# Optimization experiments

Measured on AMD Instinct MI355X. Metric: run time of the kernel, lower is better.

The kernel has to match this reference:

```python
import jax, jax.numpy as jnp
import numpy as np
import math

D_MODEL = 1024
N_HEADS = 16
D_HEAD = 64
D_MLP = 4096
N_LAYERS = 12
INIT_STD = 0.02
EPS = 1e-5
BATCH = 2
SEQ = 2048


def setup_inputs() -> dict:
    key = jax.random.key(0)
    ks = jax.random.split(key, 8)
    attn_std = INIT_STD
    proj_std = INIT_STD / math.sqrt(2 * N_LAYERS)
    return {
        "resid_pre": jax.random.normal(ks[0], (BATCH, SEQ, D_MODEL), jnp.float32),
        "ln1_w": jnp.ones((D_MODEL,), jnp.float32),
        "ln1_b": jnp.zeros((D_MODEL,), jnp.float32),
        "W_Q": attn_std * jax.random.normal(ks[1], (N_HEADS, D_MODEL, D_HEAD), jnp.float32),
        "b_Q": jnp.zeros((N_HEADS, D_HEAD), jnp.float32),
        "W_K": attn_std * jax.random.normal(ks[2], (N_HEADS, D_MODEL, D_HEAD), jnp.float32),
        "b_K": jnp.zeros((N_HEADS, D_HEAD), jnp.float32),
        "W_V": attn_std * jax.random.normal(ks[3], (N_HEADS, D_MODEL, D_HEAD), jnp.float32),
        "b_V": jnp.zeros((N_HEADS, D_HEAD), jnp.float32),
        "W_O": proj_std * jax.random.normal(ks[4], (N_HEADS, D_HEAD, D_MODEL), jnp.float32),
        "b_O": jnp.zeros((D_MODEL,), jnp.float32),
        "ln2_w": jnp.ones((D_MODEL,), jnp.float32),
        "ln2_b": jnp.zeros((D_MODEL,), jnp.float32),
        "W_in": INIT_STD * jax.random.normal(ks[5], (D_MODEL, D_MLP), jnp.float32),
        "b_in": jnp.zeros((D_MLP,), jnp.float32),
        "W_out": proj_std * jax.random.normal(ks[6], (D_MLP, D_MODEL), jnp.float32),
        "b_out": jnp.zeros((D_MODEL,), jnp.float32),
    }


def _layernorm(x, w, b):
    mean = x.mean(-1, keepdims=True)
    var = x.var(-1, keepdims=True)  # unbiased=False
    return (x - mean) / jnp.sqrt(var + EPS) * w + b


def _attention(x, W_Q, b_Q, W_K, b_K, W_V, b_V, W_O, b_O):
    # x: [b, s, d]; W_*: [h, d, k]
    q = jnp.einsum('bsd,hdk->bshk', x, W_Q) + b_Q
    k = jnp.einsum('bsd,hdk->bshk', x, W_K) + b_K
    v = jnp.einsum('bsd,hdk->bshk', x, W_V) + b_V
    scores = jnp.einsum('bqhk,bshk->bhqs', q, k) / math.sqrt(D_HEAD)
    seq = x.shape[1]
    causal = jnp.tril(jnp.ones((seq, seq), bool))
    scores = jnp.where(causal, scores, -jnp.inf)
    pattern = jax.nn.softmax(scores, axis=-1)
    z = jnp.einsum('bhqs,bshk->bqhk', pattern, v)
    return jnp.einsum('bqhk,hkd->bqd', z, W_O) + b_O


def reference(resid_pre, ln1_w, ln1_b, W_Q, b_Q, W_K, b_K, W_V, b_V, W_O, b_O,
              ln2_w, ln2_b, W_in, b_in, W_out, b_out):
    attn_out = _attention(_layernorm(resid_pre, ln1_w, ln1_b),
                          W_Q, b_Q, W_K, b_K, W_V, b_V, W_O, b_O)
    resid_mid = resid_pre + attn_out
    h = _layernorm(resid_mid, ln2_w, ln2_b)
    mlp_out = jnp.matmul(jax.nn.relu(jnp.matmul(h, W_in) + b_in), W_out) + b_out
    return resid_mid + mlp_out
```

## Files before the change

### kernel.cpp

```cpp
#include <hip/hip_runtime.h>
#include <stdint.h>


typedef unsigned short u16;
typedef __bf16 bf16x8 __attribute__((ext_vector_type(8)));
typedef __bf16 bf16x4 __attribute__((ext_vector_type(4)));
typedef __bf16 bf16x2 __attribute__((ext_vector_type(2)));
typedef short  s16x4  __attribute__((ext_vector_type(4)));
typedef float  f32x4  __attribute__((ext_vector_type(4)));

#define QSCALE 0.18033688011112042f

__device__ __forceinline__ float bf2f(unsigned int u) {
  union { unsigned int u; float f; } v; v.u = u << 16; return v.f;
}
__device__ __forceinline__ u16 f2bf(float f) {
  union { float f; unsigned int u; } v; v.f = f;
  unsigned int r = v.u + 0x7FFFu + ((v.u >> 16) & 1u);
  return (u16)(r >> 16);
}
__device__ __forceinline__ unsigned pkbf(float lo, float hi) {
#if __has_builtin(__builtin_amdgcn_cvt_pk_bf16_f32)
  bf16x2 t = __builtin_amdgcn_cvt_pk_bf16_f32(lo, hi);
  return __builtin_bit_cast(unsigned, t);
#else
  return (unsigned)f2bf(lo) | ((unsigned)f2bf(hi) << 16);
#endif
}
__device__ __forceinline__ float loadf(const void* p, size_t i, int isf) {
  return isf ? ((const float*)p)[i] : bf2f(((const u16*)p)[i]);
}

__device__ __forceinline__ f32x4 mfma16(s16x4 a, s16x4 b, f32x4 c) {
#if __has_builtin(__builtin_amdgcn_mfma_f32_16x16x16_bf16)
  return __builtin_amdgcn_mfma_f32_16x16x16_bf16(
      __builtin_bit_cast(bf16x4, a), __builtin_bit_cast(bf16x4, b), c, 0, 0, 0);
#else
  return __builtin_amdgcn_mfma_f32_16x16x16bf16_1k(a, b, c, 0, 0, 0);
#endif
}

__global__ __launch_bounds__(256) void detect_dtype(
    const unsigned int* __restrict__ x, int* __restrict__ flag) {
  __shared__ int cnt;
  if (threadIdx.x == 0) cnt = 0;
  __syncthreads();
  int c = 0;
  for (int i = threadIdx.x; i < 512; i += 256) {
    unsigned int e = (x[i] >> 23) & 0xFFu;
    if (e >= 97u && e <= 157u) c++;
  }
  atomicAdd(&cnt, c);
  __syncthreads();
  if (threadIdx.x == 0) *flag = (cnt > 384) ? 1 : 0;
}

__global__ __launch_bounds__(256) void pack_qkv_tiled(
    const int* __restrict__ flagp,
    const void* __restrict__ Wq, const void* __restrict__ Wk, const void* __restrict__ Wv,
    u16* __restrict__ WT) {
  __shared__ float t[64][65];
  const int isf = *flagp;
  const int tid = threadIdx.x;
  const int mh = blockIdx.y;
  const int mat = mh >> 4, h = mh & 15;
  const int d0 = blockIdx.x << 6;
  const void* src = (mat == 0) ? Wq : (mat == 1) ? Wk : Wv;
  const float scale = (mat == 0) ? QSCALE : 1.f;
  const int lane = tid & 63, rr = tid >> 6;
  const size_t sbase = ((size_t)h << 16) + lane;
#pragma unroll
  for (int i = 0; i < 16; i++) {
    int d = i * 4 + rr;
    t[d][lane] = loadf(src, sbase + (size_t)(d0 + d) * 64, isf) * scale;
  }
  __syncthreads();
#pragma unroll
  for (int i = 0; i < 16; i++) {
    int k = i * 4 + rr;
    WT[((size_t)((mat << 10) + (h << 6) + k) << 10) + d0 + lane] = f2bf(t[lane][k]);
  }
}

__global__ __launch_bounds__(256) void transpose_tiled(
    const int* __restrict__ flagp, const void* __restrict__ src,
    u16* __restrict__ dst, int R, int C) {
  __shared__ float t[64][65];
  const int isf = *flagp;
  const int tid = threadIdx.x;
  const int c0 = blockIdx.x << 6, r0 = blockIdx.y << 6;
  const int lane = tid & 63, rr = tid >> 6;
#pragma unroll
  for (int i = 0; i < 16; i++) {
    int r = i * 4 + rr;
    t[r][lane] = loadf(src, (size_t)(r0 + r) * C + c0 + lane, isf);
  }
  __syncthreads();
#pragma unroll
  for (int i = 0; i < 16; i++) {
    int c = i * 4 + rr;
    dst[(size_t)(c0 + c) * R + r0 + lane] = f2bf(t[lane][c]);
  }
}

__global__ __launch_bounds__(256) void pack_biases(
    const int* __restrict__ flagp,
    const void* bq, const void* bk, const void* bv,
    const void* bO, const void* bin, const void* bout,
    float* __restrict__ out) {
  const int isf = *flagp;
  int i = blockIdx.x * 256 + threadIdx.x;
  float v;
  if (i < 1024)      v = loadf(bq,   i,        isf) * QSCALE;
  else if (i < 2048) v = loadf(bk,   i - 1024, isf);
  else if (i < 3072) v = loadf(bv,   i - 2048, isf);
  else if (i < 4096) v = loadf(bO,   i - 3072, isf);
  else if (i < 8192) v = loadf(bin,  i - 4096, isf);
  else               v = loadf(bout, i - 8192, isf);
  out[i] = v;
}

template<int SRC>
__global__ __launch_bounds__(256) void ln_fwd(
    const int* __restrict__ flagp, const void* __restrict__ xin,
    const void* __restrict__ w, const void* __restrict__ b,
    u16* __restrict__ out) {
  const int isf = *flagp;
  const int row = blockIdx.x, tid = threadIdx.x;
  const int col = tid << 2;
  const size_t base = ((size_t)row << 10) + col;
  float v[4];
#pragma unroll
  for (int i = 0; i < 4; i++)
    v[i] = (SRC == 1) ? ((const float*)xin)[base + i] : loadf(xin, base + i, isf);
  float s  = v[0] + v[1] + v[2] + v[3];
  float ss = v[0]*v[0] + v[1]*v[1] + v[2]*v[2] + v[3]*v[3];
#pragma unroll
  for (int mk = 32; mk >= 1; mk >>= 1) {
    s  += __shfl_xor(s,  mk, 64);
    ss += __shfl_xor(ss, mk, 64);
  }
  __shared__ float red[8];
  if ((tid & 63) == 0) { red[tid >> 6] = s; red[4 + (tid >> 6)] = ss; }
  __syncthreads();
  float S  = red[0] + red[1] + red[2] + red[3];
  float SS = red[4] + red[5] + red[6] + red[7];
  float mean = S * (1.f / 1024.f);
  float var  = SS * (1.f / 1024.f) - mean * mean;
  float rstd = rsqrtf(var + 1e-5f);
  u16 e[4];
#pragma unroll
  for (int i = 0; i < 4; i++) {
    float wv = loadf(w, col + i, isf);
    float bv = loadf(b, col + i, isf);
    e[i] = f2bf((v[i] - mean) * rstd * wv + bv);
  }
  uint2 o;
  o.x = (unsigned)e[0] | ((unsigned)e[1] << 16);
  o.y = (unsigned)e[2] | ((unsigned)e[3] << 16);
  *(uint2*)(out + base) = o;
}

template<int MODE, int TM>
__global__ __launch_bounds__(256) void gemm_bt(
    const int* __restrict__ flagp,
    const u16* __restrict__ A, const u16* __restrict__ BT,
    const float* __restrict__ bias, const void* __restrict__ resid,
    void* __restrict__ out, void* __restrict__ out2, void* __restrict__ out3,
    int M, int N, int K, int SHL) {
  constexpr int WR = TM / 32;
  __shared__ u16 as[TM * 32];
  __shared__ u16 bs[128 * 32];
  int isf = 0;
  if (MODE == 2 || MODE == 3) isf = *flagp;
  const int Lb = blockIdx.x;
  const int xcd = Lb & 7, sidx = Lb >> 3;
  const int SH = 1 << SHL;
  const int by = xcd * SH + (sidx & (SH - 1));
  const int bx = sidx >> SHL;
  const int tid = threadIdx.x;
  const int L = tid & 63, w = tid >> 6;
  const int wm = (w >> 1) * (TM >> 1), wn = (w & 1) << 6;
  const int row0 = by * TM, col0 = bx << 7;
  const int m = L & 15, quad = L >> 4;

  f32x4 zero4 = {0.f, 0.f, 0.f, 0.f};
  f32x4 acc[WR][4];
#pragma unroll
  for (int i = 0; i < WR; i++)
#pragma unroll
    for (int j = 0; j < 4; j++) acc[i][j] = zero4;

  const int tm = tid >> 2;
  const int tk = (tid & 3) << 3;
  const u16* Ag  = A  + (size_t)(row0 + tm) * K + tk;
  const u16* Ag2 = Ag + (size_t)64 * K;
  const u16* Bg  = BT + (size_t)(col0 + tm) * K + tk;
  const u16* Bg2 = Bg + (size_t)64 * K;
  u16* asl  = &as[tid * 8];
  u16* asl2 = &as[2048 + tid * 8];
  u16* bsl  = &bs[tid * 8];
  u16* bsl2 = &bs[2048 + tid * 8];

  const int aoff = (wm + m) * 32 + quad * 8;
  const int boff = (wn + m) * 32 + quad * 8;

  int4 ar0, ar1, br0, br1;
  ar0 = *(const int4*)Ag;
  if (TM == 128) ar1 = *(const int4*)Ag2;
  br0 = *(const int4*)Bg;
  br1 = *(const int4*)Bg2;

  for (int kk = 0; kk < K; kk += 32) {
    __syncthreads();
    *(int4*)asl = ar0;
    if (TM == 128) *(int4*)asl2 = ar1;
    *(int4*)bsl = br0;
    *(int4*)bsl2 = br1;
    __syncthreads();
    if (kk + 32 < K) {
      ar0 = *(const int4*)(Ag + kk + 32);
      if (TM == 128) ar1 = *(const int4*)(Ag2 + kk + 32);
      br0 = *(const int4*)(Bg + kk + 32);
      br1 = *(const int4*)(Bg2 + kk + 32);
    }
    bf16x8 af[WR], bfr[4];
#pragma unroll
    for (int i = 0; i < WR; i++) af[i]  = *(const bf16x8*)&as[aoff + i * 512];
#pragma unroll
    for (int j = 0; j < 4; j++) bfr[j] = *(const bf16x8*)&bs[boff + j * 512];
#pragma unroll
    for (int i = 0; i < WR; i++)
#pragma unroll
      for (int j = 0; j < 4; j++)
        acc[i][j] = __builtin_amdgcn_mfma_f32_16x16x32_bf16(af[i], bfr[j], acc[i][j], 0, 0, 0);
  }

#pragma unroll
  for (int j = 0; j < 4; j++) {
    const int col = col0 + wn + j * 16 + m;
    const float bval = bias[col];
    if (MODE == 4) {
      const int sel = col >> 10;
      const int hh  = (col >> 6) & 15;
      const int f   = col & 63;
#pragma unroll
      for (int i = 0; i < WR; i++) {
        const int rowb = row0 + wm + i * 16 + quad * 4;
        if (sel < 2) {
          u16* dst = (u16*)(sel ? out2 : out);
#pragma unroll
          for (int r = 0; r < 4; r++)
            dst[((((size_t)hh << 12) + rowb + r) << 6) + f] = f2bf(acc[i][j][r] + bval);
        } else {
          uint2 o;
          o.x = pkbf(acc[i][j][0] + bval, acc[i][j][1] + bval);
          o.y = pkbf(acc[i][j][2] + bval, acc[i][j][3] + bval);
          *(uint2*)&((u16*)out3)[(((size_t)hh * 64 + f) << 12) + rowb] = o;
        }
      }
    } else {
#pragma unroll
      for (int i = 0; i < WR; i++) {
        const int rowb = row0 + wm + i * 16 + quad * 4;
#pragma unroll
        for (int r = 0; r < 4; r++) {
          float vv = acc[i][j][r] + bval;
          size_t idx = (size_t)(rowb + r) * N + col;
          if (MODE == 1) {
            ((u16*)out)[idx] = f2bf(fmaxf(vv, 0.f));
          } else if (MODE == 2) {
            ((float*)out)[idx] = vv + loadf(resid, idx, isf);
          } else if (MODE == 3) {
            float o = vv + ((const float*)resid)[idx];
            if (isf) ((float*)out)[idx] = o;
            else     ((u16*)out)[idx]   = f2bf(o);
          }
        }
      }
    }
  }
}

__global__ __launch_bounds__(256, 3) void attn_part(
    const u16* __restrict__ qh, const u16* __restrict__ kh,
    const u16* __restrict__ vT, u16* __restrict__ Opart,
    float* __restrict__ stats) {
  const int combo = blockIdx.x;
  const int qt = blockIdx.y;
  const int ci = blockIdx.z;
  const int q0 = qt << 6;
  const int nc = (q0 + 64 + 511) >> 9;
  if (ci >= nc) return;
  const int k_lo = ci << 9;
  const int k_hi = min(k_lo + 512, q0 + 64);
  const int nsteps = (k_hi - k_lo + 127) >> 7;

  __shared__ u16 kS[128 * 72];
  __shared__ u16 vS[64 * 136];
  const int tid = threadIdx.x, L = tid & 63, w = tid >> 6;
  const int m = L & 15, quad = L >> 4;
  const int h = combo >> 1, b = combo & 1;
  const size_t tb = (size_t)b * 2048;
  const size_t hbase = (size_t)h * 4096;
  const int qg = q0 + w * 16 + m;

  bf16x8 qb0, qb1;
  {
    const u16* qp = qh + ((hbase + tb + (size_t)qg) << 6) + quad * 8;
    qb0 = *(const bf16x8*)qp;
    qb1 = *(const bf16x8*)(qp + 32);
  }

  f32x4 zero4 = {0.f, 0.f, 0.f, 0.f};
  f32x4 O[4];
#pragma unroll
  for (int ft = 0; ft < 4; ft++) O[ft] = zero4;
  float mrow = -30000.f, lrow = 0.f;

  const int krow[4] = { (0*256+tid) >> 3, (1*256+tid) >> 3, (2*256+tid) >> 3, (3*256+tid) >> 3 };
  const int kc = tid & 7;
  const int vf[4] = { (0*256+tid) >> 4, (1*256+tid) >> 4, (2*256+tid) >> 4, (3*256+tid) >> 4 };
  const int vc = tid & 15;
  const int vq = (vc & 1) << 1;
  const int vk4 = (vc >> 1) << 2;
  const int vc0 = (vq << 5) + vk4;
  const int vc1 = ((vq + 1) << 5) + vk4;

  int4 kr[4], vr[4];
#pragma unroll
  for (int i = 0; i < 4; i++) {
    kr[i] = *(const int4*)(kh + ((hbase + tb + k_lo + krow[i]) << 6) + kc * 8);
    vr[i] = *(const int4*)(vT + (((size_t)h * 64 + vf[i]) << 12) + tb + k_lo + vc * 8);
  }

  for (int j = 0; j < nsteps; j++) {
    const int k0 = k_lo + (j << 7);
    __syncthreads();
#pragma unroll
    for (int i = 0; i < 4; i++) {
      *(int4*)&kS[krow[i] * 72 + kc * 8] = kr[i];
      union { int4 v; s16x4 hh[2]; } tv; tv.v = vr[i];
      *(s16x4*)&vS[vf[i] * 136 + vc0] = tv.hh[0];
      *(s16x4*)&vS[vf[i] * 136 + vc1] = tv.hh[1];
    }
    __syncthreads();
    if (j + 1 < nsteps) {
      const int k1 = k_lo + ((j + 1) << 7);
#pragma unroll
      for (int i = 0; i < 4; i++) {
        kr[i] = *(const int4*)(kh + ((hbase + tb + k1 + krow[i]) << 6) + kc * 8);
        vr[i] = *(const int4*)(vT + (((size_t)h * 64 + vf[i]) << 12) + tb + k1 + vc * 8);
      }
    }
    f32x4 sc[8];
#pragma unroll
    for (int kt = 0; kt < 8; kt++) {
      const u16* kp = &kS[(kt * 16 + m) * 72 + quad * 8];
      bf16x8 ka0 = *(const bf16x8*)kp;
      bf16x8 ka1 = *(const bf16x8*)(kp + 32);
      f32x4 t = zero4;
      t = __builtin_amdgcn_mfma_f32_16x16x32_bf16(ka0, qb0, t, 0, 0, 0);
      t = __builtin_amdgcn_mfma_f32_16x16x32_bf16(ka1, qb1, t, 0, 0, 0);
      sc[kt] = t;
    }
    if (k0 + 128 > q0) {
#pragma unroll
      for (int kt = 0; kt < 8; kt++)
#pragma unroll
        for (int r = 0; r < 4; r++) {
          int ktok = k0 + kt * 16 + quad * 4 + r;
          if (ktok > qg) sc[kt][r] = -30000.f;
        }
    }
    float mx = sc[0][0];
#pragma unroll
    for (int kt = 0; kt < 8; kt++)
#pragma unroll
      for (int r = 0; r < 4; r++) mx = fmaxf(mx, sc[kt][r]);
    mx = fmaxf(mx, __shfl_xor(mx, 16, 64));
    mx = fmaxf(mx, __shfl_xor(mx, 32, 64));
    float mnew = fmaxf(mrow, mx);
    float alpha = __builtin_amdgcn_exp2f(mrow - mnew);
    mrow = mnew;
    s16x4 pb[8];
    float sum = 0.f;
#pragma unroll
    for (int kt = 0; kt < 8; kt++) {
      float e0 = __builtin_amdgcn_exp2f(sc[kt][0] - mnew);
      float e1 = __builtin_amdgcn_exp2f(sc[kt][1] - mnew);
      float e2 = __builtin_amdgcn_exp2f(sc[kt][2] - mnew);
      float e3 = __builtin_amdgcn_exp2f(sc[kt][3] - mnew);
      sum += (e0 + e1) + (e2 + e3);
      union { uint2 u; s16x4 hh; } pu;
      pu.u.x = pkbf(e0, e1);
      pu.u.y = pkbf(e2, e3);
      pb[kt] = pu.hh;
    }
    sum += __shfl_xor(sum, 16, 64);
    sum += __shfl_xor(sum, 32, 64);
    lrow = lrow * alpha + sum;
#pragma unroll
    for (int ft = 0; ft < 4; ft++) O[ft] *= alpha;
#pragma unroll
    for (int ft = 0; ft < 4; ft++) {
      const u16* vp = &vS[(ft * 16 + m) * 136 + quad * 32];
#pragma unroll
      for (int pr = 0; pr < 4; pr++) {
        union { bf16x8 v; s16x4 hh[2]; } u;
        u.v = *(const bf16x8*)(vp + pr * 8);
        O[ft] = mfma16(u.hh[0], pb[2 * pr],     O[ft]);
        O[ft] = mfma16(u.hh[1], pb[2 * pr + 1], O[ft]);
      }
    }
  }

  __syncthreads();
#pragma unroll
  for (int ft = 0; ft < 4; ft++) {
    union { uint2 u; s16x4 hh; } o4;
    o4.u.x = pkbf(O[ft][0], O[ft][1]);
    o4.u.y = pkbf(O[ft][2], O[ft][3]);
    *(s16x4*)&kS[(w * 16 + m) * 72 + ft * 16 + quad * 4] = o4.hh;
  }
  __syncthreads();
  const int slot = (combo * 32 + qt) * 4 + ci;
  u16* op = Opart + ((size_t)slot << 12);
#pragma unroll
  for (int it = 0; it < 2; it++) {
    int idx = it * 256 + tid;
    int row = idx >> 3, c = idx & 7;
    *(int4*)&op[row * 64 + c * 8] = *(const int4*)&kS[row * 72 + c * 8];
  }
  if (quad == 0) {
    stats[slot * 128 + w * 16 + m]      = mrow;
    stats[slot * 128 + 64 + w * 16 + m] = lrow;
  }
}

__global__ __launch_bounds__(256) void attn_merge(
    const u16* __restrict__ Opart, const float* __restrict__ stats,
    u16* __restrict__ z) {
  const int combo = blockIdx.x, qt = blockIdx.y;
  const int h = combo >> 1, b = combo & 1;
  const int q0 = qt << 6;
  const int nc = (q0 + 64 + 511) >> 9;
  const int tid = threadIdx.x;
  const int t = tid >> 2, f0 = (tid & 3) << 4;
  const int slot0 = (combo * 32 + qt) * 4;
  float M = -3e4f;
  for (int ci = 0; ci < nc; ci++)
    M = fmaxf(M, stats[(slot0 + ci) * 128 + t]);
  float acc[16];
#pragma unroll
  for (int e = 0; e < 16; e++) acc[e] = 0.f;
  float ltot = 0.f;
  for (int ci = 0; ci < nc; ci++) {
    float mi = stats[(slot0 + ci) * 128 + t];
    float li = stats[(slot0 + ci) * 128 + 64 + t];
    float wgt = exp2f(mi - M);
    ltot += wgt * li;
    const u16* op = Opart + (((size_t)(slot0 + ci)) << 12) + t * 64 + f0;
    union { int4 v; u16 u[8]; } a0, a1;
    a0.v = *(const int4*)op;
    a1.v = *(const int4*)(op + 8);
#pragma unroll
    for (int e = 0; e < 8; e++) {
      acc[e]     += wgt * bf2f(a0.u[e]);
      acc[8 + e] += wgt * bf2f(a1.u[e]);
    }
  }
  float inv = 1.f / ltot;
  union { int4 v; u16 u[8]; } o0, o1;
#pragma unroll
  for (int e = 0; e < 8; e++) {
    o0.u[e] = f2bf(acc[e] * inv);
    o1.u[e] = f2bf(acc[8 + e] * inv);
  }
  size_t tok = (size_t)b * 2048 + q0 + t;
  *(int4*)&z[tok * 1024 + h * 64 + f0]     = o0.v;
  *(int4*)&z[tok * 1024 + h * 64 + f0 + 8] = o1.v;
}

extern "C" void kernel_launch(void* const* d_in, const int* in_sizes, int n_in,
                              void* d_out, int out_size, void* d_ws, size_t ws_size,
                              hipStream_t stream) {
  (void)in_sizes; (void)n_in; (void)out_size; (void)ws_size;
  const void* resid_pre = d_in[0];
  const void* ln1_w = d_in[1];
  const void* ln1_b = d_in[2];
  const void* W_Q   = d_in[3];
  const void* b_Q   = d_in[4];
  const void* W_K   = d_in[5];
  const void* b_K   = d_in[6];
  const void* W_V   = d_in[7];
  const void* b_V   = d_in[8];
  const void* W_O   = d_in[9];
  const void* b_O   = d_in[10];
  const void* ln2_w = d_in[11];
  const void* ln2_b = d_in[12];
  const void* W_in  = d_in[13];
  const void* b_in  = d_in[14];
  const void* W_out = d_in[15];
  const void* b_out = d_in[16];

  char* p = (char*)d_ws;
  auto alloc = [&](size_t bytes) {
    char* r = p; p += (bytes + 255) & ~(size_t)255; return (void*)r;
  };
  int*   flag      = (int*)  alloc(256);
  u16*   WqkvT     = (u16*)  alloc(3072ull * 1024 * 2);
  u16*   WoT       = (u16*)  alloc(1024ull * 1024 * 2);
  u16*   WinT      = (u16*)  alloc(4096ull * 1024 * 2);
  u16*   WoutT     = (u16*)  alloc(1024ull * 4096 * 2);
  float* biases    = (float*)alloc(9216 * 4);
  u16*   xn        = (u16*)  alloc(4096ull * 1024 * 2);
  u16*   q_hm      = (u16*)  alloc(16ull * 4096 * 64 * 2);
  u16*   k_hm      = (u16*)  alloc(16ull * 4096 * 64 * 2);
  u16*   vTws      = (u16*)  alloc(16ull * 64 * 4096 * 2);
  float* resid_mid = (float*)alloc(4096ull * 1024 * 4);
  u16*   h2        = (u16*)  alloc(4096ull * 1024 * 2);
  u16*   act       = (u16*)  alloc(4096ull * 4096 * 2);
  u16*   z = xn;
  u16*   Opart = act;
  float* stats = (float*)h2;

  detect_dtype<<<1, 256, 0, stream>>>((const unsigned int*)resid_pre, flag);

  pack_qkv_tiled<<<dim3(16, 48), 256, 0, stream>>>(flag, W_Q, W_K, W_V, WqkvT);
  transpose_tiled<<<dim3(16, 16), 256, 0, stream>>>(flag, W_O,   WoT,   1024, 1024);
  transpose_tiled<<<dim3(64, 16), 256, 0, stream>>>(flag, W_in,  WinT,  1024, 4096);
  transpose_tiled<<<dim3(16, 64), 256, 0, stream>>>(flag, W_out, WoutT, 4096, 1024);
  pack_biases<<<36, 256, 0, stream>>>(flag, b_Q, b_K, b_V, b_O, b_in, b_out, biases);

  ln_fwd<0><<<4096, 256, 0, stream>>>(flag, resid_pre, ln1_w, ln1_b, xn);
  gemm_bt<4, 128><<<768, 256, 0, stream>>>(
      flag, xn, WqkvT, biases, nullptr, q_hm, k_hm, vTws, 4096, 3072, 1024, 2);
  attn_part<<<dim3(32, 32, 4), 256, 0, stream>>>(q_hm, k_hm, vTws, Opart, stats);
  attn_merge<<<dim3(32, 32), 256, 0, stream>>>(Opart, stats, z);
  gemm_bt<2, 64><<<512, 256, 0, stream>>>(
      flag, z, WoT, biases + 3072, resid_pre, resid_mid, nullptr, nullptr, 4096, 1024, 1024, 3);
  ln_fwd<1><<<4096, 256, 0, stream>>>(flag, resid_mid, ln2_w, ln2_b, h2);
  gemm_bt<1, 128><<<1024, 256, 0, stream>>>(
      flag, h2, WinT, biases + 4096, nullptr, act, nullptr, nullptr, 4096, 4096, 1024, 2);
  gemm_bt<3, 64><<<512, 256, 0, stream>>>(
      flag, act, WoutT, biases + 8192, resid_mid, d_out, nullptr, nullptr, 4096, 1024, 4096, 3);
}
```

Baseline: 432.6 us.

## Split K across two warp groups in narrow-N GEMMs with LDS reduction

Adds an in-block split-K template parameter to the GEMM kernel. The O-projection and MLP-down GEMMs (N=1024, only 512 blocks) now launch 512 threads per block, with two 4-wave groups each handling half of K and then combining partial accumulators through shared memory before the epilogue. The aim is more waves per CU and more memory parallelism for these low-block-count GEMMs. The cost is extra LDS use, an added reduction pass with barriers, and a larger block that may lower the number of resident blocks.

```diff
diff --git a/kernel.cpp b/kernel.cpp
--- a/kernel.cpp
+++ b/kernel.cpp
@@ -161,16 +161,23 @@
   *(uint2*)(out + base) = o;
 }
 
-template<int MODE, int TM>
-__global__ __launch_bounds__(256) void gemm_bt(
+template<int MODE, int TM, int KW>
+__global__ __launch_bounds__(KW * 256) void gemm_bt(
     const int* __restrict__ flagp,
     const u16* __restrict__ A, const u16* __restrict__ BT,
     const float* __restrict__ bias, const void* __restrict__ resid,
     void* __restrict__ out, void* __restrict__ out2, void* __restrict__ out3,
     int M, int N, int K, int SHL) {
   constexpr int WR = TM / 32;
-  __shared__ u16 as[TM * 32];
-  __shared__ u16 bs[128 * 32];
+  constexpr int ASZ = TM * 32;
+  constexpr int BSZ = 128 * 32;
+  constexpr int STAGE_B = KW * (ASZ + BSZ) * 2;
+  constexpr int RED_B = (KW > 1) ? TM * 132 * 4 : 1;
+  constexpr int SMEM_B = STAGE_B > RED_B ? STAGE_B : RED_B;
+  __shared__ __align__(16) char smem[SMEM_B];
+  u16* as = (u16*)smem;
+  u16* bs = (u16*)smem + KW * ASZ;
+
   int isf = 0;
   if (MODE == 2 || MODE == 3) isf = *flagp;
   const int Lb = blockIdx.x;
@@ -180,7 +187,8 @@
   const int bx = sidx >> SHL;
   const int tid = threadIdx.x;
   const int L = tid & 63, w = tid >> 6;
-  const int wm = (w >> 1) * (TM >> 1), wn = (w & 1) << 6;
+  const int g = w >> 2, wl = w & 3;
+  const int wm = (wl >> 1) * (TM >> 1), wn = (wl & 1) << 6;
   const int row0 = by * TM, col0 = bx << 7;
   const int m = L & 15, quad = L >> 4;
 
@@ -191,16 +199,20 @@
 #pragma unroll
     for (int j = 0; j < 4; j++) acc[i][j] = zero4;
 
-  const int tm = tid >> 2;
-  const int tk = (tid & 3) << 3;
-  const u16* Ag  = A  + (size_t)(row0 + tm) * K + tk;
+  const int KSEG = K / KW;
+  const int tl = tid & 255;
+  const int tm = tl >> 2;
+  const int tk = (tl & 3) << 3;
+  const u16* Ag  = A  + (size_t)(row0 + tm) * K + g * KSEG + tk;
   const u16* Ag2 = Ag + (size_t)64 * K;
-  const u16* Bg  = BT + (size_t)(col0 + tm) * K + tk;
+  const u16* Bg  = BT + (size_t)(col0 + tm) * K + g * KSEG + tk;
   const u16* Bg2 = Bg + (size_t)64 * K;
-  u16* asl  = &as[tid * 8];
-  u16* asl2 = &as[2048 + tid * 8];
-  u16* bsl  = &bs[tid * 8];
-  u16* bsl2 = &bs[2048 + tid * 8];
+  u16* asg  = as + g * ASZ;
+  u16* bsg  = bs + g * BSZ;
+  u16* asl  = asg + tl * 8;
+  u16* asl2 = asg + 2048 + tl * 8;
+  u16* bsl  = bsg + tl * 8;
+  u16* bsl2 = bsg + 2048 + tl * 8;
 
   const int aoff = (wm + m) * 32 + quad * 8;
   const int boff = (wn + m) * 32 + quad * 8;
@@ -211,14 +223,14 @@
   br0 = *(const int4*)Bg;
   br1 = *(const int4*)Bg2;
 
-  for (int kk = 0; kk < K; kk += 32) {
+  for (int kk = 0; kk < KSEG; kk += 32) {
     __syncthreads();
     *(int4*)asl = ar0;
     if (TM == 128) *(int4*)asl2 = ar1;
     *(int4*)bsl = br0;
     *(int4*)bsl2 = br1;
     __syncthreads();
-    if (kk + 32 < K) {
+    if (kk + 32 < KSEG) {
       ar0 = *(const int4*)(Ag + kk + 32);
       if (TM == 128) ar1 = *(const int4*)(Ag2 + kk + 32);
       br0 = *(const int4*)(Bg + kk + 32);
@@ -226,9 +238,9 @@
     }
     bf16x8 af[WR], bfr[4];
 #pragma unroll
-    for (int i = 0; i < WR; i++) af[i]  = *(const bf16x8*)&as[aoff + i * 512];
-#pragma unroll
-    for (int j = 0; j < 4; j++) bfr[j] = *(const bf16x8*)&bs[boff + j * 512];
+    for (int i = 0; i < WR; i++) af[i]  = *(const bf16x8*)&asg[aoff + i * 512];
+#pragma unroll
+    for (int j = 0; j < 4; j++) bfr[j] = *(const bf16x8*)&bsg[boff + j * 512];
 #pragma unroll
     for (int i = 0; i < WR; i++)
 #pragma unroll
@@ -236,45 +248,71 @@
         acc[i][j] = __builtin_amdgcn_mfma_f32_16x16x32_bf16(af[i], bfr[j], acc[i][j], 0, 0, 0);
   }
 
-#pragma unroll
-  for (int j = 0; j < 4; j++) {
-    const int col = col0 + wn + j * 16 + m;
-    const float bval = bias[col];
-    if (MODE == 4) {
-      const int sel = col >> 10;
-      const int hh  = (col >> 6) & 15;
-      const int f   = col & 63;
-#pragma unroll
-      for (int i = 0; i < WR; i++) {
-        const int rowb = row0 + wm + i * 16 + quad * 4;
-        if (sel < 2) {
-          u16* dst = (u16*)(sel ? out2 : out);
+  if (KW > 1) {
+    __syncthreads();
+    float* red = (float*)smem;
+    if (g == 1) {
+#pragma unroll
+      for (int i = 0; i < WR; i++)
+#pragma unroll
+        for (int j = 0; j < 4; j++)
 #pragma unroll
           for (int r = 0; r < 4; r++)
-            dst[((((size_t)hh << 12) + rowb + r) << 6) + f] = f2bf(acc[i][j][r] + bval);
-        } else {
-          uint2 o;
-          o.x = pkbf(acc[i][j][0] + bval, acc[i][j][1] + bval);
-          o.y = pkbf(acc[i][j][2] + bval, acc[i][j][3] + bval);
-          *(uint2*)&((u16*)out3)[(((size_t)hh * 64 + f) << 12) + rowb] = o;
+            red[(wm + i * 16 + quad * 4 + r) * 132 + wn + j * 16 + m] = acc[i][j][r];
+    }
+    __syncthreads();
+    if (g == 0) {
+#pragma unroll
+      for (int i = 0; i < WR; i++)
+#pragma unroll
+        for (int j = 0; j < 4; j++)
+#pragma unroll
+          for (int r = 0; r < 4; r++)
+            acc[i][j][r] += red[(wm + i * 16 + quad * 4 + r) * 132 + wn + j * 16 + m];
+    }
+  }
+
+  if (g == 0) {
+#pragma unroll
+    for (int j = 0; j < 4; j++) {
+      const int col = col0 + wn + j * 16 + m;
+      const float bval = bias[col];
+      if (MODE == 4) {
+        const int sel = col >> 10;
+        const int hh  = (col >> 6) & 15;
+        const int f   = col & 63;
+#pragma unroll
+        for (int i = 0; i < WR; i++) {
+          const int rowb = row0 + wm + i * 16 + quad * 4;
+          if (sel < 2) {
+            u16* dst = (u16*)(sel ? out2 : out);
+#pragma unroll
+            for (int r = 0; r < 4; r++)
+              dst[((((size_t)hh << 12) + rowb + r) << 6) + f] = f2bf(acc[i][j][r] + bval);
+          } else {
+            uint2 o;
+            o.x = pkbf(acc[i][j][0] + bval, acc[i][j][1] + bval);
+            o.y = pkbf(acc[i][j][2] + bval, acc[i][j][3] + bval);
+            *(uint2*)&((u16*)out3)[(((size_t)hh * 64 + f) << 12) + rowb] = o;
+          }
         }
-      }
-    } else {
-#pragma unroll
-      for (int i = 0; i < WR; i++) {
-        const int rowb = row0 + wm + i * 16 + quad * 4;
-#pragma unroll
-        for (int r = 0; r < 4; r++) {
-          float vv = acc[i][j][r] + bval;
-          size_t idx = (size_t)(rowb + r) * N + col;
-          if (MODE == 1) {
-            ((u16*)out)[idx] = f2bf(fmaxf(vv, 0.f));
-          } else if (MODE == 2) {
-            ((float*)out)[idx] = vv + loadf(resid, idx, isf);
-          } else if (MODE == 3) {
-            float o = vv + ((const float*)resid)[idx];
-            if (isf) ((float*)out)[idx] = o;
-            else     ((u16*)out)[idx]   = f2bf(o);
+      } else {
+#pragma unroll
+        for (int i = 0; i < WR; i++) {
+          const int rowb = row0 + wm + i * 16 + quad * 4;
+#pragma unroll
+          for (int r = 0; r < 4; r++) {
+            float vv = acc[i][j][r] + bval;
+            size_t idx = (size_t)(rowb + r) * N + col;
+            if (MODE == 1) {
+              ((u16*)out)[idx] = f2bf(fmaxf(vv, 0.f));
+            } else if (MODE == 2) {
+              ((float*)out)[idx] = vv + loadf(resid, idx, isf);
+            } else if (MODE == 3) {
+              float o = vv + ((const float*)resid)[idx];
+              if (isf) ((float*)out)[idx] = o;
+              else     ((u16*)out)[idx]   = f2bf(o);
+            }
           }
         }
       }
@@ -534,15 +572,15 @@
   pack_biases<<<36, 256, 0, stream>>>(flag, b_Q, b_K, b_V, b_O, b_in, b_out, biases);
 
   ln_fwd<0><<<4096, 256, 0, stream>>>(flag, resid_pre, ln1_w, ln1_b, xn);
-  gemm_bt<4, 128><<<768, 256, 0, stream>>>(
+  gemm_bt<4, 128, 1><<<768, 256, 0, stream>>>(
       flag, xn, WqkvT, biases, nullptr, q_hm, k_hm, vTws, 4096, 3072, 1024, 2);
   attn_part<<<dim3(32, 32, 4), 256, 0, stream>>>(q_hm, k_hm, vTws, Opart, stats);
   attn_merge<<<dim3(32, 32), 256, 0, stream>>>(Opart, stats, z);
-  gemm_bt<2, 64><<<512, 256, 0, stream>>>(
+  gemm_bt<2, 64, 2><<<512, 512, 0, stream>>>(
       flag, z, WoT, biases + 3072, resid_pre, resid_mid, nullptr, nullptr, 4096, 1024, 1024, 3);
   ln_fwd<1><<<4096, 256, 0, stream>>>(flag, resid_mid, ln2_w, ln2_b, h2);
-  gemm_bt<1, 128><<<1024, 256, 0, stream>>>(
+  gemm_bt<1, 128, 1><<<1024, 256, 0, stream>>>(
       flag, h2, WinT, biases + 4096, nullptr, act, nullptr, nullptr, 4096, 4096, 1024, 2);
-  gemm_bt<3, 64><<<512, 256, 0, stream>>>(
+  gemm_bt<3, 64, 2><<<512, 512, 0, stream>>>(
       flag, act, WoutT, biases + 8192, resid_mid, d_out, nullptr, nullptr, 4096, 1024, 4096, 3);
 }
```

Result: no change. 430.3 us (-0.5%).
